# Performance work log

Hardware: AMD Instinct MI355X
Metric: run time of the kernel (lower is better)

## Reference

```python
import math
import jax, jax.numpy as jnp
import numpy as np

LENGTHS = [1024, 768, 512, 1024, 256, 896, 640, 512]  # ragged seq lens, sum = 5632
NEG = -10000.0  # mask fill value used by the torch module


def setup_inputs() -> dict:
    key = jax.random.key(0)
    k1, k2 = jax.random.split(key)
    total = int(sum(LENGTHS))  # 5632 packed tokens
    H, HKV, D = 16, 4, 64      # GQA: 16 query heads, 4 kv heads
    q = jax.random.normal(k1, (total, H, D), dtype=jnp.float32)
    kv = jax.random.normal(k2, (total, 2, HKV, D), dtype=jnp.float32)
    cu_seqlens = jnp.asarray(np.concatenate([[0], np.cumsum(LENGTHS)]), dtype=jnp.int32)
    return {"q": q, "kv": kv, "cu_seqlens": cu_seqlens, "max_seqlen": 1024}


def _varlen_attention(q, kv, cu_seqlens, max_seqlen):
    # GQA repeat: '... hkv d -> ... (hkv g) d' == repeat each kv head g times
    g = q.shape[1] // kv.shape[2]
    kv = jnp.repeat(kv, g, axis=2)
    k, v = kv[:, 0], kv[:, 1]            # [total, H, D]

    starts = cu_seqlens[:-1]
    lens = cu_seqlens[1:] - starts       # [B]
    S = max_seqlen
    pos = jnp.arange(S)
    gather_idx = starts[:, None] + pos[None, :]          # [B, S]
    key_mask = pos[None, :] < lens[:, None]              # [B, S] True = valid
    gather_idx = jnp.where(key_mask, gather_idx, 0)

    m = key_mask[:, :, None, None]
    # pad ragged tokens into dense [B, S, H, D] buffers (zeros where invalid)
    qp = jnp.where(m, q[gather_idx], 0.0)
    kp = jnp.where(m, k[gather_idx], 0.0)
    vp = jnp.where(m, v[gather_idx], 0.0)

    scale = 1.0 / math.sqrt(q.shape[-1])
    scores = jnp.einsum('bthd,bshd->bhts', qp, kp * scale)   # [B, H, S, S]
    # key padding mask: 0 on valid keys, -10000 on padded keys
    scores = scores + jnp.where(key_mask, 0.0, NEG)[:, None, None, :]
    # causal mask: triu(-10000, 1)
    scores = scores + jnp.triu(jnp.full((S, S), NEG, dtype=scores.dtype), 1)

    attn = jax.nn.softmax(scores, axis=-1)
    out_padded = jnp.einsum('bhts,bshd->bthd', attn, vp)     # [B, S, H, D]

    # unpad back to packed [total, H, D]
    tok = jnp.arange(q.shape[0])
    b = jnp.searchsorted(cu_seqlens, tok, side='right') - 1  # batch id per token
    s = tok - starts[b]                                      # position within seq
    return out_padded[b, s]


def reference(q, kv, cu_seqlens, max_seqlen):
    return _varlen_attention(q, kv, cu_seqlens, max_seqlen)
```

## Files before the change

kernel.cpp:

```cpp
#include <hip/hip_runtime.h>


#define H    16
#define HKV  4
#define D    64
#define BM   32
#define NEGF (-1e30f)

using bf8 = __attribute__((ext_vector_type(8))) short;
using f4v = __attribute__((ext_vector_type(4))) float;
typedef unsigned int u32;

union bf8u { bf8 v; u32 w[4]; };

__device__ inline u32 pk(float a, float b) {
    union { float f; u32 u; } x, y; x.f = a; y.f = b;
    return __builtin_amdgcn_perm(y.u + 0x8000u, x.u + 0x8000u, 0x07060302u);
}

#define MFMA(A, B, C) __builtin_amdgcn_mfma_f32_16x16x32_bf16(A, B, C, 0, 0, 0)

__global__ __launch_bounds__(256)
void preconv7(const float* __restrict__ kv, short* __restrict__ Kb,
              short* __restrict__ Vb, int ntiles)
{
    __shared__ __attribute__((aligned(16))) float Vs[64 * 68];

    const int T = blockIdx.x, kvh = blockIdx.y, t = threadIdx.x;
    const int lane = t & 63, fi = t >> 6;
    const int qd = lane >> 4, c = lane & 15;
    const size_t tbase = ((size_t)kvh * ntiles + T) * 8;

    #pragma unroll
    for (int i = 0; i < 4; ++i) {
        int r = (t >> 4) + 16 * i, col = (t & 15) * 4;
        float4 v = *(const float4*)&kv[(size_t)(64 * T + r) * 512 + (HKV + kvh) * 64 + col];
        *(float4*)&Vs[r * 68 + col] = v;
    }

    #pragma unroll
    for (int ff = 0; ff < 2; ++ff) {
        const int f = fi + 4 * ff, ki = f >> 1, dc = f & 1;
        const int tok = 64 * T + ki * 16 + c;
        const float* p = kv + (size_t)tok * 512 + kvh * 64 + dc * 32 + qd * 8;
        float4 a = *(const float4*)p, b = *(const float4*)(p + 4);
        uint4 o = make_uint4(pk(a.x, a.y), pk(a.z, a.w), pk(b.x, b.y), pk(b.z, b.w));
        *(uint4*)&Kb[((tbase + f) * 64 + lane) * 8] = o;
    }

    __syncthreads();

    #pragma unroll
    for (int ff = 0; ff < 2; ++ff) {
        const int f = fi + 4 * ff, di = f >> 1, kc = f & 1;
        float v[8];
        #pragma unroll
        for (int j = 0; j < 8; ++j) v[j] = Vs[(kc * 32 + qd * 8 + j) * 68 + di * 16 + c];
        uint4 o = make_uint4(pk(v[0], v[1]), pk(v[2], v[3]), pk(v[4], v[5]), pk(v[6], v[7]));
        *(uint4*)&Vb[((tbase + f) * 64 + lane) * 8] = o;
    }
}

__global__ __launch_bounds__(256, 2)
void attn7(const float* __restrict__ q, const short* __restrict__ Kb,
           const short* __restrict__ Vb, const int* __restrict__ cu,
           float* __restrict__ out, int nb, int ntiles)
{
    __shared__ __attribute__((aligned(16))) short Ps[4][2 * BM / 2 * 72];

    const int kvh = blockIdx.y;

    int bid = blockIdx.x, b = -1, start = 0, len = 0, q0 = 0, acc = 0;
    for (int i = 0; i < nb; ++i) {
        int s0 = cu[i], l = cu[i + 1] - s0, nt = (l + BM - 1) / BM;
        if (bid < acc + nt) { b = i; start = s0; len = l; q0 = (nt - 1 - (bid - acc)) * BM; break; }
        acc += nt;
    }
    if (b < 0) return;

    const int t = threadIdx.x, w = t >> 6, lane = t & 63;
    const int qd = lane >> 4, c = lane & 15;
    const int h = kvh * 4 + w;
    const int rows = min(BM, len - q0), kend = q0 + rows;
    const int niter = (kend + 63) >> 6;
    const float SC = 0.125f * 1.44269504f;

    bf8u qf[2][2];
    #pragma unroll
    for (int s = 0; s < 2; ++s) {
        int qr = min(16 * s + c, rows - 1);
        const float* qp = q + (size_t)(start + q0 + qr) * (H * D) + h * D + qd * 8;
        float4 a0 = *(const float4*)qp;
        float4 a1 = *(const float4*)(qp + 4);
        float4 a2 = *(const float4*)(qp + 32);
        float4 a3 = *(const float4*)(qp + 36);
        qf[s][0].w[0] = pk(a0.x * SC, a0.y * SC); qf[s][0].w[1] = pk(a0.z * SC, a0.w * SC);
        qf[s][0].w[2] = pk(a1.x * SC, a1.y * SC); qf[s][0].w[3] = pk(a1.z * SC, a1.w * SC);
        qf[s][1].w[0] = pk(a2.x * SC, a2.y * SC); qf[s][1].w[1] = pk(a2.z * SC, a2.w * SC);
        qf[s][1].w[2] = pk(a3.x * SC, a3.y * SC); qf[s][1].w[3] = pk(a3.z * SC, a3.w * SC);
    }

    const size_t htile = (size_t)kvh * ntiles + (start >> 6);
    const short* kp0 = Kb + (htile * 8 * 64 + lane) * 8;
    const short* vp0 = Vb + (htile * 8 * 64 + lane) * 8;

    float l_i[2] = {0.f, 0.f};
    f4v o[2][4];
    #pragma unroll
    for (int s = 0; s < 2; ++s)
        #pragma unroll
        for (int d = 0; d < 4; ++d) o[s][d] = (f4v){0, 0, 0, 0};

    short* Psw = &Ps[w][0];

    bf8 kc_[4][2];
    #pragma unroll
    for (int ki = 0; ki < 4; ++ki) {
        kc_[ki][0] = *(const bf8*)(kp0 + (ki * 2 + 0) * 512);
        kc_[ki][1] = *(const bf8*)(kp0 + (ki * 2 + 1) * 512);
    }

    for (int it = 0; it < niter; ++it) {
        const short* vp = vp0 + (size_t)it * 4096;
        bf8 vf[4][2];
        #pragma unroll
        for (int di = 0; di < 4; ++di) {
            vf[di][0] = *(const bf8*)(vp + (di * 2 + 0) * 512);
            vf[di][1] = *(const bf8*)(vp + (di * 2 + 1) * 512);
        }
        const short* kp = kp0 + (size_t)min(it + 1, niter - 1) * 4096;
        bf8 kn_[4][2];
        #pragma unroll
        for (int ki = 0; ki < 4; ++ki) {
            kn_[ki][0] = *(const bf8*)(kp + (ki * 2 + 0) * 512);
            kn_[ki][1] = *(const bf8*)(kp + (ki * 2 + 1) * 512);
        }

        f4v s0[4], s1[4];
        #pragma unroll
        for (int ki = 0; ki < 4; ++ki) {
            f4v z = {0, 0, 0, 0};
            z = MFMA(kc_[ki][0], qf[0][0].v, z);
            s0[ki] = MFMA(kc_[ki][1], qf[0][1].v, z);
            f4v y = {0, 0, 0, 0};
            y = MFMA(kc_[ki][0], qf[1][0].v, y);
            s1[ki] = MFMA(kc_[ki][1], qf[1][1].v, y);
        }

        const int kt0 = 64 * it;
        bf8 p[2][2];
        #pragma unroll
        for (int s = 0; s < 2; ++s) {
            float e[16];
            #pragma unroll
            for (int ki = 0; ki < 4; ++ki)
                #pragma unroll
                for (int r = 0; r < 4; ++r)
                    e[4 * ki + r] = s ? s1[ki][r] : s0[ki][r];
            if (kt0 + 63 > q0 + 16 * s) {
                const int limit = q0 + 16 * s + c - kt0;
                #pragma unroll
                for (int ki = 0; ki < 4; ++ki)
                    #pragma unroll
                    for (int r = 0; r < 4; ++r)
                        if (16 * ki + 4 * qd + r > limit) e[4 * ki + r] = NEGF;
            }
            float ls = 0.f;
            #pragma unroll
            for (int i = 0; i < 16; ++i) { e[i] = exp2f(e[i]); ls += e[i]; }
            l_i[s] += ls;
            short* Pss = Psw + s * 16 * 72;
            #pragma unroll
            for (int j = 0; j < 4; ++j) {
                u32 lo = pk(e[4 * j], e[4 * j + 1]), hi = pk(e[4 * j + 2], e[4 * j + 3]);
                *(uint2*)&Pss[c * 72 + 16 * j + 4 * qd] = make_uint2(lo, hi);
            }
            p[s][0] = *(const bf8*)&Pss[c * 72 + qd * 8];
            p[s][1] = *(const bf8*)&Pss[c * 72 + 32 + qd * 8];
        }

        #pragma unroll
        for (int di = 0; di < 4; ++di) {
            o[0][di] = MFMA(vf[di][0], p[0][0], o[0][di]);
            o[0][di] = MFMA(vf[di][1], p[0][1], o[0][di]);
            o[1][di] = MFMA(vf[di][0], p[1][0], o[1][di]);
            o[1][di] = MFMA(vf[di][1], p[1][1], o[1][di]);
        }

        #pragma unroll
        for (int ki = 0; ki < 4; ++ki) { kc_[ki][0] = kn_[ki][0]; kc_[ki][1] = kn_[ki][1]; }
    }

    #pragma unroll
    for (int s = 0; s < 2; ++s) {
        if (16 * s + c < rows) {
            float lt = l_i[s] + __shfl_xor(l_i[s], 16, 64);
            lt += __shfl_xor(lt, 32, 64);
            const float inv = 1.f / lt;
            float* op = out + (size_t)(start + q0 + 16 * s + c) * (H * D) + h * D + 4 * qd;
            *(float4*)(op)      = make_float4(o[s][0][0] * inv, o[s][0][1] * inv, o[s][0][2] * inv, o[s][0][3] * inv);
            *(float4*)(op + 16) = make_float4(o[s][1][0] * inv, o[s][1][1] * inv, o[s][1][2] * inv, o[s][1][3] * inv);
            *(float4*)(op + 32) = make_float4(o[s][2][0] * inv, o[s][2][1] * inv, o[s][2][2] * inv, o[s][2][3] * inv);
            *(float4*)(op + 48) = make_float4(o[s][3][0] * inv, o[s][3][1] * inv, o[s][3][2] * inv, o[s][3][3] * inv);
        }
    }
}

extern "C" void kernel_launch(void* const* d_in, const int* in_sizes, int n_in,
                              void* d_out, int out_size, void* d_ws, size_t ws_size,
                              hipStream_t stream) {
    const float* q  = (const float*)d_in[0];
    const float* kv = (const float*)d_in[1];
    const int*   cu = (const int*)d_in[2];
    float* out = (float*)d_out;

    const int total  = in_sizes[0] / (H * D);
    const int nb     = in_sizes[2] - 1;
    const int ntiles = (total + 63) / 64;

    short* Kb = (short*)d_ws;
    short* Vb = Kb + (size_t)HKV * ntiles * 8 * 64 * 8;

    dim3 gridA(ntiles, HKV);
    preconv7<<<gridA, 256, 0, stream>>>(kv, Kb, Vb, ntiles);

    const int tile_ub = total / BM + nb;
    dim3 gridB(tile_ub, HKV);
    attn7<<<gridB, 256, 0, stream>>>(q, Kb, Vb, cu, out, nb, ntiles);
}
```

Baseline: 117.5 us.

## Split long causal query tiles into KV chunks with a separate bf16 partial reduce

Each 32-row query tile is split along the key dimension into 256-key chunks, so long tiles become several blocks. Partial unnormalized outputs go to workspace in bf16 with their row sums, and a third reduce kernel sums and normalizes them. Tiles with a single chunk still write directly. Occupancy goes from 2 to 4 blocks per CU and the K register prefetch is dropped. The aim is to fix load imbalance across the causal triangle, at the cost of an extra launch, workspace traffic and bf16 rounding of partial outputs.

Result: slower. 155.5 us (+32.4%).

```diff
diff --git a/kernel.cpp b/kernel.cpp
--- a/kernel.cpp
+++ b/kernel.cpp
@@ -20,12 +20,16 @@
 
 #define MFMA(A, B, C) __builtin_amdgcn_mfma_f32_16x16x32_bf16(A, B, C, 0, 0, 0)
 
+__device__ __host__ inline int chunk_prefix(int n) {
+    int k = n >> 3, r = n & 7;
+    return n + 4 * k * (k - 1) + r * k;
+}
+
 __global__ __launch_bounds__(256)
-void preconv7(const float* __restrict__ kv, short* __restrict__ Kb,
-              short* __restrict__ Vb, int ntiles)
+void preconv8(const float* __restrict__ kv, short* __restrict__ Kb,
+              short* __restrict__ Vb, int ntiles, int total)
 {
     __shared__ __attribute__((aligned(16))) float Vs[64 * 68];
-
     const int T = blockIdx.x, kvh = blockIdx.y, t = threadIdx.x;
     const int lane = t & 63, fi = t >> 6;
     const int qd = lane >> 4, c = lane & 15;
@@ -34,22 +38,20 @@
     #pragma unroll
     for (int i = 0; i < 4; ++i) {
         int r = (t >> 4) + 16 * i, col = (t & 15) * 4;
-        float4 v = *(const float4*)&kv[(size_t)(64 * T + r) * 512 + (HKV + kvh) * 64 + col];
+        int tok = min(64 * T + r, total - 1);
+        float4 v = *(const float4*)&kv[(size_t)tok * 512 + (HKV + kvh) * 64 + col];
         *(float4*)&Vs[r * 68 + col] = v;
     }
-
     #pragma unroll
     for (int ff = 0; ff < 2; ++ff) {
         const int f = fi + 4 * ff, ki = f >> 1, dc = f & 1;
-        const int tok = 64 * T + ki * 16 + c;
+        const int tok = min(64 * T + ki * 16 + c, total - 1);
         const float* p = kv + (size_t)tok * 512 + kvh * 64 + dc * 32 + qd * 8;
         float4 a = *(const float4*)p, b = *(const float4*)(p + 4);
         uint4 o = make_uint4(pk(a.x, a.y), pk(a.z, a.w), pk(b.x, b.y), pk(b.z, b.w));
         *(uint4*)&Kb[((tbase + f) * 64 + lane) * 8] = o;
     }
-
     __syncthreads();
-
     #pragma unroll
     for (int ff = 0; ff < 2; ++ff) {
         const int f = fi + 4 * ff, di = f >> 1, kc = f & 1;
@@ -61,28 +63,45 @@
     }
 }
 
-__global__ __launch_bounds__(256, 2)
-void attn7(const float* __restrict__ q, const short* __restrict__ Kb,
+__global__ __launch_bounds__(256, 4)
+void attn8(const float* __restrict__ q, const short* __restrict__ Kb,
            const short* __restrict__ Vb, const int* __restrict__ cu,
-           float* __restrict__ out, int nb, int ntiles)
+           float* __restrict__ out, short* __restrict__ OW, float* __restrict__ LW,
+           int nb, int ntiles, int ubs)
 {
-    __shared__ __attribute__((aligned(16))) short Ps[4][2 * BM / 2 * 72];
+    __shared__ __attribute__((aligned(16))) short Ps[4][BM * 72];
 
     const int kvh = blockIdx.y;
-
-    int bid = blockIdx.x, b = -1, start = 0, len = 0, q0 = 0, acc = 0;
-    for (int i = 0; i < nb; ++i) {
-        int s0 = cu[i], l = cu[i + 1] - s0, nt = (l + BM - 1) / BM;
-        if (bid < acc + nt) { b = i; start = s0; len = l; q0 = (nt - 1 - (bid - acc)) * BM; break; }
-        acc += nt;
+    const int bid = blockIdx.x;
+
+    int b = -1, start = 0, len = 0, tt = 0, ch = 0;
+    {
+        int acc = 0;
+        for (int i = 0; i < nb; ++i) {
+            int s0 = cu[i], l = cu[i + 1] - s0, nt = (l + BM - 1) / BM;
+            int S = chunk_prefix(nt);
+            if (bid < acc + S) {
+                int j = bid - acc;
+                for (int kk = 0;; ++kk) {
+                    int tin = min(8, nt - 8 * kk), gs = tin * (kk + 1);
+                    if (j < gs) { tt = 8 * kk + j / (kk + 1); ch = j % (kk + 1); break; }
+                    j -= gs;
+                }
+                b = i; start = s0; len = l; break;
+            }
+            acc += S;
+        }
     }
     if (b < 0) return;
 
     const int t = threadIdx.x, w = t >> 6, lane = t & 63;
     const int qd = lane >> 4, c = lane & 15;
     const int h = kvh * 4 + w;
+    const int q0 = BM * tt;
     const int rows = min(BM, len - q0), kend = q0 + rows;
-    const int niter = (kend + 63) >> 6;
+    const int ct = (tt >> 3) + 1;
+    const int kts = 256 * ch, kte = min(256 * (ch + 1), kend);
+    const int niter = (kte - kts + 63) >> 6;
     const float SC = 0.125f * 1.44269504f;
 
     bf8u qf[2][2];
@@ -110,44 +129,36 @@
     for (int s = 0; s < 2; ++s)
         #pragma unroll
         for (int d = 0; d < 4; ++d) o[s][d] = (f4v){0, 0, 0, 0};
-
     short* Psw = &Ps[w][0];
 
-    bf8 kc_[4][2];
-    #pragma unroll
-    for (int ki = 0; ki < 4; ++ki) {
-        kc_[ki][0] = *(const bf8*)(kp0 + (ki * 2 + 0) * 512);
-        kc_[ki][1] = *(const bf8*)(kp0 + (ki * 2 + 1) * 512);
-    }
-
     for (int it = 0; it < niter; ++it) {
-        const short* vp = vp0 + (size_t)it * 4096;
-        bf8 vf[4][2];
+        const int kt0 = kts + 64 * it;
+        const short* kp = kp0 + (size_t)(kt0 >> 6) * 4096;
+        const short* vp = vp0 + (size_t)(kt0 >> 6) * 4096;
+
+        bf8 kf[4][2], vf[4][2];
+        #pragma unroll
+        for (int ki = 0; ki < 4; ++ki) {
+            kf[ki][0] = *(const bf8*)(kp + (ki * 2 + 0) * 512);
+            kf[ki][1] = *(const bf8*)(kp + (ki * 2 + 1) * 512);
+        }
         #pragma unroll
         for (int di = 0; di < 4; ++di) {
             vf[di][0] = *(const bf8*)(vp + (di * 2 + 0) * 512);
             vf[di][1] = *(const bf8*)(vp + (di * 2 + 1) * 512);
         }
-        const short* kp = kp0 + (size_t)min(it + 1, niter - 1) * 4096;
-        bf8 kn_[4][2];
-        #pragma unroll
-        for (int ki = 0; ki < 4; ++ki) {
-            kn_[ki][0] = *(const bf8*)(kp + (ki * 2 + 0) * 512);
-            kn_[ki][1] = *(const bf8*)(kp + (ki * 2 + 1) * 512);
-        }
 
         f4v s0[4], s1[4];
         #pragma unroll
         for (int ki = 0; ki < 4; ++ki) {
             f4v z = {0, 0, 0, 0};
-            z = MFMA(kc_[ki][0], qf[0][0].v, z);
-            s0[ki] = MFMA(kc_[ki][1], qf[0][1].v, z);
+            z = MFMA(kf[ki][0], qf[0][0].v, z);
+            s0[ki] = MFMA(kf[ki][1], qf[0][1].v, z);
             f4v y = {0, 0, 0, 0};
-            y = MFMA(kc_[ki][0], qf[1][0].v, y);
-            s1[ki] = MFMA(kc_[ki][1], qf[1][1].v, y);
-        }
-
-        const int kt0 = 64 * it;
+            y = MFMA(kf[ki][0], qf[1][0].v, y);
+            s1[ki] = MFMA(kf[ki][1], qf[1][1].v, y);
+        }
+
         bf8 p[2][2];
         #pragma unroll
         for (int s = 0; s < 2; ++s) {
@@ -186,23 +197,94 @@
             o[1][di] = MFMA(vf[di][0], p[1][0], o[1][di]);
             o[1][di] = MFMA(vf[di][1], p[1][1], o[1][di]);
         }
-
-        #pragma unroll
-        for (int ki = 0; ki < 4; ++ki) { kc_[ki][0] = kn_[ki][0]; kc_[ki][1] = kn_[ki][1]; }
-    }
-
-    #pragma unroll
-    for (int s = 0; s < 2; ++s) {
-        if (16 * s + c < rows) {
+    }
+
+    if (ct == 1) {
+        #pragma unroll
+        for (int s = 0; s < 2; ++s) {
             float lt = l_i[s] + __shfl_xor(l_i[s], 16, 64);
             lt += __shfl_xor(lt, 32, 64);
-            const float inv = 1.f / lt;
-            float* op = out + (size_t)(start + q0 + 16 * s + c) * (H * D) + h * D + 4 * qd;
-            *(float4*)(op)      = make_float4(o[s][0][0] * inv, o[s][0][1] * inv, o[s][0][2] * inv, o[s][0][3] * inv);
-            *(float4*)(op + 16) = make_float4(o[s][1][0] * inv, o[s][1][1] * inv, o[s][1][2] * inv, o[s][1][3] * inv);
-            *(float4*)(op + 32) = make_float4(o[s][2][0] * inv, o[s][2][1] * inv, o[s][2][2] * inv, o[s][2][3] * inv);
-            *(float4*)(op + 48) = make_float4(o[s][3][0] * inv, o[s][3][1] * inv, o[s][3][2] * inv, o[s][3][3] * inv);
-        }
+            if (16 * s + c < rows) {
+                const float inv = 1.f / lt;
+                float* op = out + (size_t)(start + q0 + 16 * s + c) * (H * D) + h * D + 4 * qd;
+                #pragma unroll
+                for (int di = 0; di < 4; ++di)
+                    *(float4*)(op + 16 * di) = make_float4(o[s][di][0] * inv, o[s][di][1] * inv,
+                                                           o[s][di][2] * inv, o[s][di][3] * inv);
+            }
+        }
+    } else {
+        const size_t slot = (size_t)kvh * ubs + bid;
+        short* op = OW + slot * 8192 + w * 2048;
+        float* lp = LW + slot * 128 + w * 32;
+        #pragma unroll
+        for (int s = 0; s < 2; ++s) {
+            float lt = l_i[s] + __shfl_xor(l_i[s], 16, 64);
+            lt += __shfl_xor(lt, 32, 64);
+            if (qd == 0) lp[16 * s + c] = lt;
+            #pragma unroll
+            for (int di = 0; di < 4; ++di) {
+                u32 lo = pk(o[s][di][0], o[s][di][1]), hi = pk(o[s][di][2], o[s][di][3]);
+                *(uint2*)&op[(16 * s + c) * 64 + 16 * di + 4 * qd] = make_uint2(lo, hi);
+            }
+        }
+    }
+}
+
+__global__ __launch_bounds__(256, 4)
+void reduce8(const short* __restrict__ OW, const float* __restrict__ LW,
+             const int* __restrict__ cu, float* __restrict__ out,
+             int nb, int ubs)
+{
+    const int kvh = blockIdx.y;
+    int bid = blockIdx.x, b = -1, start = 0, len = 0, tt = 0, sacc = 0;
+    {
+        int acc = 0;
+        for (int i = 0; i < nb; ++i) {
+            int s0 = cu[i], l = cu[i + 1] - s0, nt = (l + BM - 1) / BM;
+            if (bid < acc + nt) { b = i; start = s0; len = l; tt = bid - acc; break; }
+            acc += nt; sacc += chunk_prefix(nt);
+        }
+    }
+    if (b < 0) return;
+    const int ct = (tt >> 3) + 1;
+    if (ct == 1) return;
+    const int sbase = sacc + chunk_prefix(tt);
+
+    const int w = threadIdx.x >> 6, lane = threadIdx.x & 63;
+    const int r_ = lane >> 1, dh = (lane & 1) * 32;
+    const int rows = min(BM, len - BM * tt);
+
+    float acc32[32];
+    #pragma unroll
+    for (int j = 0; j < 32; ++j) acc32[j] = 0.f;
+    float lsum = 0.f;
+
+    for (int chk = 0; chk < ct; ++chk) {
+        const size_t slot = (size_t)kvh * ubs + sbase + chk;
+        const short* op = OW + slot * 8192 + w * 2048 + r_ * 64 + dh;
+        lsum += LW[slot * 128 + w * 32 + r_];
+        #pragma unroll
+        for (int j = 0; j < 4; ++j) {
+            uint4 u = *(const uint4*)(op + 8 * j);
+            const u32 uu[4] = {u.x, u.y, u.z, u.w};
+            #pragma unroll
+            for (int m = 0; m < 4; ++m) {
+                union { u32 q; float f; } lo, hi;
+                lo.q = uu[m] << 16; hi.q = uu[m] & 0xFFFF0000u;
+                acc32[8 * j + 2 * m]     += lo.f;
+                acc32[8 * j + 2 * m + 1] += hi.f;
+            }
+        }
+    }
+
+    if (r_ < rows) {
+        const float inv = 1.f / lsum;
+        float* op = out + (size_t)(start + BM * tt + r_) * (H * D) + (kvh * 4 + w) * 64 + dh;
+        #pragma unroll
+        for (int j = 0; j < 8; ++j)
+            *(float4*)(op + 4 * j) = make_float4(acc32[4 * j] * inv, acc32[4 * j + 1] * inv,
+                                                 acc32[4 * j + 2] * inv, acc32[4 * j + 3] * inv);
     }
 }
 
@@ -217,14 +299,20 @@
     const int total  = in_sizes[0] / (H * D);
     const int nb     = in_sizes[2] - 1;
     const int ntiles = (total + 63) / 64;
+    const int ntq    = total / BM + nb;
+    const int ubs    = chunk_prefix(ntq);
 
     short* Kb = (short*)d_ws;
-    short* Vb = Kb + (size_t)HKV * ntiles * 8 * 64 * 8;
+    short* Vb = Kb + (size_t)HKV * ntiles * 4096;
+    short* OW = Vb + (size_t)HKV * ntiles * 4096;
+    float* LW = (float*)(OW + (size_t)HKV * ubs * 8192);
 
     dim3 gridA(ntiles, HKV);
-    preconv7<<<gridA, 256, 0, stream>>>(kv, Kb, Vb, ntiles);
-
-    const int tile_ub = total / BM + nb;
-    dim3 gridB(tile_ub, HKV);
-    attn7<<<gridB, 256, 0, stream>>>(q, Kb, Vb, cu, out, nb, ntiles);
-}
+    preconv8<<<gridA, 256, 0, stream>>>(kv, Kb, Vb, ntiles, total);
+
+    dim3 gridB(ubs, HKV);
+    attn8<<<gridB, 256, 0, stream>>>(q, Kb, Vb, cu, out, OW, LW, nb, ntiles, ubs);
+
+    dim3 gridC(ntq, HKV);
+    reduce8<<<gridC, 256, 0, stream>>>(OW, LW, cu, out, nb, ubs);
+}
```
